# Kernel tuning notes

Hardware: AMD Instinct MI355X
Metric: run time of the kernel (lower is better)

The kernel has to match this reference:

```python
import jax, jax.numpy as jnp
import numpy as np

MARGIN_POS = 0.0
MARGIN_NEG = 1.0
NUM_CLASSES = 1000


def setup_inputs() -> dict:
    key = jax.random.key(0)
    k1, k2, k3, k4, k5 = jax.random.split(key, 5)
    B, D, M = 1024, 512, 32768
    R = M - B  # memory bank length after dedup/truncate
    embeddings = jax.random.normal(k1, (B, D), dtype=jnp.float32)
    labels = jax.random.randint(k2, (B,), 0, NUM_CLASSES).astype(jnp.int64)
    emb_mem = jax.random.normal(k3, (R, D), dtype=jnp.float32)
    # offset so memory labels are disjoint from batch labels (torch.isin dedup is a no-op)
    lbl_mem = (jax.random.randint(k4, (R,), 0, NUM_CLASSES) + NUM_CLASSES).astype(jnp.int64)
    add_to_mem = jax.random.randint(k5, (B,), 0, 2).astype(bool)
    return {"embeddings": embeddings, "labels": labels, "emb_mem": emb_mem,
            "lbl_mem": lbl_mem, "add_to_mem": add_to_mem}


def _loss(embeddings, labels, emb_mem, lbl_mem):
    B = embeddings.shape[0]
    # reference set = detached batch embeddings ++ memory bank (both are constants w.r.t. grad)
    ref_e = jax.lax.stop_gradient(jnp.concatenate([embeddings, emb_mem], axis=0))  # [R, D]
    ref_l = jnp.concatenate([labels, lbl_mem], axis=0)                              # [R]
    idx_ref = jnp.concatenate([jnp.arange(B, dtype=labels.dtype),
                               -jnp.ones(lbl_mem.shape[0], dtype=labels.dtype)])    # [R]
    # squared L2 distance matrix [B, R] via (|a|^2 + |b|^2 - 2 a.b), clamped at 0
    sq_a = jnp.sum(embeddings * embeddings, axis=1)  # [B]
    sq_b = jnp.sum(ref_e * ref_e, axis=1)            # [R]
    d = jnp.maximum(sq_a[:, None] + sq_b[None, :] - 2.0 * (embeddings @ ref_e.T), 0.0)
    not_self = idx_ref[None, :] != jnp.arange(B, dtype=labels.dtype)[:, None]  # [B, R]
    same = labels[:, None] == ref_l[None, :]                                   # [B, R]
    loss_ap = d - MARGIN_POS
    loss_an = jnp.maximum(MARGIN_NEG - d, 0.0)
    mask_pos = same & not_self & (loss_ap > 0)
    mask_neg = (~same) & not_self & (loss_an > 0)
    eps = 1e-6
    loss_pos = (jnp.where(mask_pos, loss_ap, 0.0).sum(1)
                / (mask_pos.sum(1).astype(d.dtype) + eps)).sum()
    loss_neg = (jnp.where(mask_neg, loss_an, 0.0).sum(1)
                / (mask_neg.sum(1).astype(d.dtype) + eps)).sum()
    return (loss_pos + loss_neg) / B


def reference(embeddings, labels, emb_mem, lbl_mem, add_to_mem):
    # add_to_mem only affects the (stateful) memory-bank update, not the returned loss
    return _loss(embeddings, labels, emb_mem, lbl_mem)
```

## Files before the change

kernel.cpp:

```cpp
#include <hip/hip_runtime.h>

typedef __attribute__((ext_vector_type(8))) short short8;
typedef __attribute__((ext_vector_type(4))) float f32x4;

#define GLOAD16(g, l)                                                        \
  __builtin_amdgcn_global_load_lds(                                          \
      (const __attribute__((address_space(1))) unsigned int*)(g),            \
      (__attribute__((address_space(3))) unsigned int*)(l), 16, 0, 0)

__device__ __forceinline__ unsigned short f2bf(float f) {
  union { float f; unsigned int u; } v;
  v.f = f;
  unsigned int u = v.u;
  u += 0x7FFFu + ((u >> 16) & 1u);
  return (unsigned short)(u >> 16);
}

__device__ __forceinline__ short8 pack8(float4 a, float4 b) {
  short8 r;
  r[0] = (short)f2bf(a.x); r[1] = (short)f2bf(a.y);
  r[2] = (short)f2bf(a.z); r[3] = (short)f2bf(a.w);
  r[4] = (short)f2bf(b.x); r[5] = (short)f2bf(b.y);
  r[6] = (short)f2bf(b.z); r[7] = (short)f2bf(b.w);
  return r;
}

#define BM 128
#define BN 128
#define BK 32

__global__ __launch_bounds__(256)
void prep2_kernel(const float* __restrict__ emb, const int* __restrict__ labels,
                  const float* __restrict__ emb_mem, const int* __restrict__ lbl_mem,
                  unsigned short* __restrict__ refbf, float* __restrict__ sqb,
                  int* __restrict__ reflab, float* __restrict__ facc,
                  int* __restrict__ fcnt, int Bn, int Dn, int Mn) {
  if (blockIdx.x == 0 && threadIdx.x == 0) { *facc = 0.f; *fcnt = 0; }
  int wid = threadIdx.x >> 6, lane = threadIdx.x & 63;
  int row = blockIdx.x * 4 + wid;
  if (row >= Mn) return;
  const float* src = (row < Bn) ? (emb + (size_t)row * Dn)
                                : (emb_mem + (size_t)(row - Bn) * Dn);
  unsigned short* dst = refbf + (size_t)row * Dn;
  float s = 0.f;
  for (int c0 = lane * 8; c0 < Dn; c0 += 64 * 8) {
    float4 v0 = ((const float4*)(src + c0))[0];
    float4 v1 = ((const float4*)(src + c0))[1];
    s += v0.x * v0.x + v0.y * v0.y + v0.z * v0.z + v0.w * v0.w;
    s += v1.x * v1.x + v1.y * v1.y + v1.z * v1.z + v1.w * v1.w;
    *(short8*)(dst + c0) = pack8(v0, v1);
  }
#pragma unroll
  for (int off = 32; off; off >>= 1) s += __shfl_xor(s, off);
  if (lane == 0) {
    sqb[row] = s;
    reflab[row] = (row < Bn) ? labels[row] : lbl_mem[row - Bn];
  }
}

__global__ __launch_bounds__(256, 2)
void gemm512x2_kernel(const unsigned short* __restrict__ refbf,
                      const float* __restrict__ sqb,
                      const int* __restrict__ reflab,
                      float* __restrict__ part) {
  __shared__ __align__(16) char smem[32768];
  unsigned short* As = (unsigned short*)smem;
  unsigned short* Bs = (unsigned short*)(smem + 8192);
  f32x4* red4 = (f32x4*)smem;

  const int npart = 128;
  int bid = blockIdx.x;
  int c = bid & 7, g = bid >> 3;
  int jp = c * 16 + (g >> 3);
  int it = g & 7;
  int rowBase = it * BM, colBase = jp * 256;

  int tid = threadIdx.x, lane = tid & 63, w = tid >> 6;
  int wr = w >> 1, wc = w & 1;
  int l16 = lane & 15, quad = lane >> 4;
  int lrow = lane >> 2, lk = lane & 3;

  int ra = w * 32 + lrow;
  int caa = (lk - (ra >> 1)) & 3;
  const char* gA0 = (const char*)refbf + (size_t)(rowBase + ra) * 1024 + caa * 16;
  const char* gA1 = gA0 + 16 * 1024;
  char* lA = (char*)As + w * 2048;
  int rb = w * 64 + lrow;
  int cab = (lk - (rb >> 1)) & 3;
  const char* gB0 = (const char*)refbf + (size_t)(colBase + rb) * 1024 + cab * 16;
  const char* gB1 = gB0 + 16 * 1024;
  const char* gB2 = gB0 + 32 * 1024;
  const char* gB3 = gB0 + 48 * 1024;
  char* lB = (char*)Bs + w * 4096;

  f32x4 acc[4][8] = {};
  for (int kk = 0; kk < 16; ++kk) {
    int ko = kk * 64;
    GLOAD16(gA0 + ko, lA);
    GLOAD16(gA1 + ko, lA + 1024);
    GLOAD16(gB0 + ko, lB);
    GLOAD16(gB1 + ko, lB + 1024);
    GLOAD16(gB2 + ko, lB + 2048);
    GLOAD16(gB3 + ko, lB + 3072);
    __syncthreads();
    short8 af[4], bfr[8];
#pragma unroll
    for (int mi = 0; mi < 4; ++mi) {
      int row = wr * 64 + mi * 16 + l16;
      af[mi] = *(const short8*)&As[row * BK + ((quad + (row >> 1)) & 3) * 8];
    }
#pragma unroll
    for (int ni = 0; ni < 8; ++ni) {
      int row = wc * 128 + ni * 16 + l16;
      bfr[ni] = *(const short8*)&Bs[row * BK + ((quad + (row >> 1)) & 3) * 8];
    }
#pragma unroll
    for (int mi = 0; mi < 4; ++mi)
#pragma unroll
      for (int ni = 0; ni < 8; ++ni)
        acc[mi][ni] = __builtin_amdgcn_mfma_f32_16x16x32_bf16(
            af[mi], bfr[ni], acc[mi][ni], 0, 0, 0);
    __syncthreads();
  }

  float sqc[8];
  int labc[8];
#pragma unroll
  for (int ni = 0; ni < 8; ++ni) {
    int gcol = colBase + wc * 128 + ni * 16 + l16;
    sqc[ni] = sqb[gcol];
    labc[ni] = reflab[gcol];
  }
#pragma unroll
  for (int mi = 0; mi < 4; ++mi) {
    int lr0 = wr * 64 + mi * 16 + quad * 4;
#pragma unroll
    for (int r = 0; r < 4; ++r) {
      int lrl = lr0 + r;
      int grow = rowBase + lrl;
      float sqr = sqb[grow];
      int labr = reflab[grow];
      float ps = 0.f, ns = 0.f, cpk = 0.f;
#pragma unroll
      for (int ni = 0; ni < 8; ++ni) {
        int gcol = colBase + wc * 128 + ni * 16 + l16;
        float dist = fmaxf(sqr + sqc[ni] - 2.0f * acc[mi][ni][r], 0.f);
        bool self = (gcol == grow);
        bool same = (labc[ni] == labr);
        if (same && !self && dist > 0.f) { ps += dist; cpk += 1.f; }
        if (!same && !self && dist < 1.f) { ns += 1.f - dist; cpk += 512.f; }
      }
      ps += __shfl_xor(ps, 8);
      ns += __shfl_xor(ns, 8);
      cpk += __shfl_xor(cpk, 8);
      if (l16 < 8) {
        f32x4 v = {ps, ns, cpk, 0.f};
        red4[(wc * BM + lrl) * 8 + l16] = v;
      }
    }
  }
  __syncthreads();
  if (tid < BM) {
    f32x4 s = {0.f, 0.f, 0.f, 0.f};
#pragma unroll
    for (int c2 = 0; c2 < 2; ++c2)
#pragma unroll
      for (int k = 0; k < 8; ++k)
        s += red4[(c2 * BM + tid) * 8 + ((k + tid) & 7)];
    float nc = floorf(s[2] * (1.0f / 512.0f));
    float pc = s[2] - 512.f * nc;
    f32x4 o = {s[0], pc, s[1], nc};
    ((f32x4*)part)[(size_t)(rowBase + tid) * npart + jp] = o;
  }
}

__global__ __launch_bounds__(256)
void gemm_generic_kernel(const unsigned short* __restrict__ refbf,
                         const float* __restrict__ sqb,
                         const int* __restrict__ reflab,
                         float* __restrict__ part,
                         int Dn, int mtiles, int ntiles) {
  __shared__ unsigned short As[BM * BK];
  __shared__ unsigned short Bs[BN * BK];
  __shared__ f32x4 redbuf4[2 * BM];

  int bid = blockIdx.x;
  int it = bid % mtiles, jt = bid / mtiles;
  int rowBase = it * BM, colBase = jt * BN;
  int tid = threadIdx.x, lane = tid & 63, w = tid >> 6;
  int wr = w >> 1, wc = w & 1;
  int l16 = lane & 15, quad = lane >> 4;
  int lrow = lane >> 2, lk = lane & 3;
  size_t rowB = (size_t)Dn * 2;
  int r0 = w * 32 + lrow;
  int ca = (lk - (r0 >> 1)) & 3;
  const char* gA0 = (const char*)refbf + (size_t)(rowBase + r0) * rowB + ca * 16;
  const char* gA1 = gA0 + 16 * rowB;
  const char* gB0 = (const char*)refbf + (size_t)(colBase + r0) * rowB + ca * 16;
  const char* gB1 = gB0 + 16 * rowB;
  char* lA = (char*)As + w * 2048;
  char* lB = (char*)Bs + w * 2048;

  f32x4 acc[4][4] = {};
  for (int k0 = 0; k0 < Dn; k0 += BK) {
    int koff = k0 * 2;
    GLOAD16(gA0 + koff, lA);
    GLOAD16(gA1 + koff, lA + 1024);
    GLOAD16(gB0 + koff, lB);
    GLOAD16(gB1 + koff, lB + 1024);
    __syncthreads();
    short8 af[4], bfr[4];
#pragma unroll
    for (int mi = 0; mi < 4; ++mi) {
      int row = wr * 64 + mi * 16 + l16;
      af[mi] = *(const short8*)&As[row * BK + ((quad + (row >> 1)) & 3) * 8];
    }
#pragma unroll
    for (int ni = 0; ni < 4; ++ni) {
      int row = wc * 64 + ni * 16 + l16;
      bfr[ni] = *(const short8*)&Bs[row * BK + ((quad + (row >> 1)) & 3) * 8];
    }
#pragma unroll
    for (int mi = 0; mi < 4; ++mi)
#pragma unroll
      for (int ni = 0; ni < 4; ++ni)
        acc[mi][ni] = __builtin_amdgcn_mfma_f32_16x16x32_bf16(
            af[mi], bfr[ni], acc[mi][ni], 0, 0, 0);
    __syncthreads();
  }

  float sqc[4];
  int labc[4];
#pragma unroll
  for (int ni = 0; ni < 4; ++ni) {
    int gcol = colBase + wc * 64 + ni * 16 + l16;
    sqc[ni] = sqb[gcol];
    labc[ni] = reflab[gcol];
  }
#pragma unroll
  for (int mi = 0; mi < 4; ++mi) {
    int lr0 = wr * 64 + mi * 16 + quad * 4;
#pragma unroll
    for (int r = 0; r < 4; ++r) {
      int lrl = lr0 + r;
      int grow = rowBase + lrl;
      float sqr = sqb[grow];
      int labr = reflab[grow];
      float ps = 0.f, pc = 0.f, ns = 0.f, nc = 0.f;
#pragma unroll
      for (int ni = 0; ni < 4; ++ni) {
        int gcol = colBase + wc * 64 + ni * 16 + l16;
        float dist = fmaxf(sqr + sqc[ni] - 2.0f * acc[mi][ni][r], 0.f);
        bool self = (gcol == grow);
        bool same = (labc[ni] == labr);
        if (same && !self && dist > 0.f) { ps += dist; pc += 1.f; }
        if (!same && !self && dist < 1.f) { ns += 1.f - dist; nc += 1.f; }
      }
#pragma unroll
      for (int off = 8; off; off >>= 1) {
        ps += __shfl_xor(ps, off);
        pc += __shfl_xor(pc, off);
        ns += __shfl_xor(ns, off);
        nc += __shfl_xor(nc, off);
      }
      if (l16 == 0) {
        f32x4 v = {ps, pc, ns, nc};
        redbuf4[wc * BM + lrl] = v;
      }
    }
  }
  __syncthreads();
  if (tid < BM) {
    f32x4 s = redbuf4[tid] + redbuf4[BM + tid];
    ((f32x4*)part)[(size_t)(rowBase + tid) * ntiles + jt] = s;
  }
}

__global__ __launch_bounds__(256)
void reduce_final_kernel(const float* __restrict__ part,
                         float* __restrict__ facc, int* __restrict__ fcnt,
                         float* __restrict__ out, int Bn, int npart) {
  __shared__ float rsum[4];
  int tid = threadIdx.x, w = tid >> 6, lane = tid & 63;
  int row = blockIdx.x * 4 + w;
  const f32x4* part4 = (const f32x4*)part;
  float rl = 0.f;
  if (row < Bn) {
    f32x4 a = {0.f, 0.f, 0.f, 0.f};
    for (int j = lane; j < npart; j += 64)
      a += part4[(size_t)row * npart + j];
#pragma unroll
    for (int off = 32; off; off >>= 1) {
      a[0] += __shfl_xor(a[0], off);
      a[1] += __shfl_xor(a[1], off);
      a[2] += __shfl_xor(a[2], off);
      a[3] += __shfl_xor(a[3], off);
    }
    rl = a[0] / (a[1] + 1e-6f) + a[2] / (a[3] + 1e-6f);
  }
  if (lane == 0) rsum[w] = rl;
  __syncthreads();
  if (tid == 0) {
    float bs = rsum[0] + rsum[1] + rsum[2] + rsum[3];
    atomicAdd(facc, bs);
    __threadfence();
    int old = atomicAdd(fcnt, 1);
    if (old == (int)gridDim.x - 1) {
      __threadfence();
      float tot = atomicAdd(facc, 0.f);
      out[0] = tot / (float)Bn;
    }
  }
}

extern "C" void kernel_launch(void* const* d_in, const int* in_sizes, int n_in,
                              void* d_out, int out_size, void* d_ws, size_t ws_size,
                              hipStream_t stream) {
  const float* emb     = (const float*)d_in[0];
  const int*   labels  = (const int*)d_in[1];
  const float* emb_mem = (const float*)d_in[2];
  const int*   lbl_mem = (const int*)d_in[3];

  int Bn = in_sizes[1];
  int Dn = in_sizes[0] / Bn;
  int Rn = in_sizes[3];
  int Mn = Bn + Rn;
  int mtiles = Bn / BM, ntiles = Mn / BN;

  char* ws = (char*)d_ws;
  unsigned short* refbf = (unsigned short*)ws;
  size_t off = (size_t)Mn * Dn * 2;
  float* sqb    = (float*)(ws + off);
  int*   reflab = (int*)(ws + off + (size_t)Mn * 4);
  float* part   = (float*)(ws + off + (size_t)Mn * 8);
  float* facc   = part + (size_t)Bn * ntiles * 4;
  int*   fcnt   = (int*)(facc + 1);

  prep2_kernel<<<(Mn + 3) / 4, 256, 0, stream>>>(
      emb, labels, emb_mem, lbl_mem, refbf, sqb, reflab, facc, fcnt, Bn, Dn, Mn);

  bool fast = (Dn == 512 && mtiles == 8 && ntiles == 256);
  if (fast) {
    gemm512x2_kernel<<<1024, 256, 0, stream>>>(refbf, sqb, reflab, part);
    reduce_final_kernel<<<(Bn + 3) / 4, 256, 0, stream>>>(
        part, facc, fcnt, (float*)d_out, Bn, 128);
  } else {
    gemm_generic_kernel<<<mtiles * ntiles, 256, 0, stream>>>(
        refbf, sqb, reflab, part, Dn, mtiles, ntiles);
    reduce_final_kernel<<<(Bn + 3) / 4, 256, 0, stream>>>(
        part, facc, fcnt, (float*)d_out, Bn, ntiles);
  }
}
```

Before: 160.2 us.

## Double-buffer LDS tiles in fast GEMM to overlap loads with MFMA

Splits the fast-path GEMM's shared memory into two buffers and prefetches the next K-slice with global_load_lds while MFMAs run on the current one. The aim is to hide global-to-LDS latency behind compute. LDS use grows to 48KB per block, which may limit occupancy, and the K loop is now fully unrolled. Correctness depends on the sync still remaining at the end of each iteration, which falls in the unshown part of the loop.

Measured after the change: 162.2 us. About the same (+1.2%).

```diff
diff --git a/kernel.cpp b/kernel.cpp
--- a/kernel.cpp
+++ b/kernel.cpp
@@ -59,13 +59,11 @@
 }
 
 __global__ __launch_bounds__(256, 2)
-void gemm512x2_kernel(const unsigned short* __restrict__ refbf,
-                      const float* __restrict__ sqb,
-                      const int* __restrict__ reflab,
-                      float* __restrict__ part) {
-  __shared__ __align__(16) char smem[32768];
-  unsigned short* As = (unsigned short*)smem;
-  unsigned short* Bs = (unsigned short*)(smem + 8192);
+void gemm512x2db_kernel(const unsigned short* __restrict__ refbf,
+                        const float* __restrict__ sqb,
+                        const int* __restrict__ reflab,
+                        float* __restrict__ part) {
+  __shared__ __align__(16) char smem[49152];
   f32x4* red4 = (f32x4*)smem;
 
   const int npart = 128;
@@ -84,35 +82,50 @@
   int caa = (lk - (ra >> 1)) & 3;
   const char* gA0 = (const char*)refbf + (size_t)(rowBase + ra) * 1024 + caa * 16;
   const char* gA1 = gA0 + 16 * 1024;
-  char* lA = (char*)As + w * 2048;
   int rb = w * 64 + lrow;
   int cab = (lk - (rb >> 1)) & 3;
   const char* gB0 = (const char*)refbf + (size_t)(colBase + rb) * 1024 + cab * 16;
   const char* gB1 = gB0 + 16 * 1024;
   const char* gB2 = gB0 + 32 * 1024;
   const char* gB3 = gB0 + 48 * 1024;
-  char* lB = (char*)Bs + w * 4096;
+
+  char* lA[2] = {smem + w * 2048, smem + 24576 + w * 2048};
+  char* lB[2] = {smem + 8192 + w * 4096, smem + 24576 + 8192 + w * 4096};
 
   f32x4 acc[4][8] = {};
+
+  GLOAD16(gA0, lA[0]);
+  GLOAD16(gA1, lA[0] + 1024);
+  GLOAD16(gB0, lB[0]);
+  GLOAD16(gB1, lB[0] + 1024);
+  GLOAD16(gB2, lB[0] + 2048);
+  GLOAD16(gB3, lB[0] + 3072);
+  __syncthreads();
+
+#pragma unroll
   for (int kk = 0; kk < 16; ++kk) {
-    int ko = kk * 64;
-    GLOAD16(gA0 + ko, lA);
-    GLOAD16(gA1 + ko, lA + 1024);
-    GLOAD16(gB0 + ko, lB);
-    GLOAD16(gB1 + ko, lB + 1024);
-    GLOAD16(gB2 + ko, lB + 2048);
-    GLOAD16(gB3 + ko, lB + 3072);
-    __syncthreads();
+    int cur = kk & 1, nxt = cur ^ 1;
+    if (kk < 15) {
+      int ko = (kk + 1) * 64;
+      GLOAD16(gA0 + ko, lA[nxt]);
+      GLOAD16(gA1 + ko, lA[nxt] + 1024);
+      GLOAD16(gB0 + ko, lB[nxt]);
+      GLOAD16(gB1 + ko, lB[nxt] + 1024);
+      GLOAD16(gB2 + ko, lB[nxt] + 2048);
+      GLOAD16(gB3 + ko, lB[nxt] + 3072);
+    }
+    const unsigned short* Asc = (const unsigned short*)(smem + cur * 24576);
+    const unsigned short* Bsc = (const unsigned short*)(smem + cur * 24576 + 8192);
     short8 af[4], bfr[8];
 #pragma unroll
     for (int mi = 0; mi < 4; ++mi) {
       int row = wr * 64 + mi * 16 + l16;
-      af[mi] = *(const short8*)&As[row * BK + ((quad + (row >> 1)) & 3) * 8];
+      af[mi] = *(const short8*)&Asc[row * BK + ((quad + (row >> 1)) & 3) * 8];
     }
 #pragma unroll
     for (int ni = 0; ni < 8; ++ni) {
       int row = wc * 128 + ni * 16 + l16;
-      bfr[ni] = *(const short8*)&Bs[row * BK + ((quad + (row >> 1)) & 3) * 8];
+      bfr[ni] = *(const short8*)&Bsc[row * BK + ((quad + (row >> 1)) & 3) * 8];
     }
 #pragma unroll
     for (int mi = 0; mi < 4; ++mi)
@@ -341,7 +354,7 @@
 
   bool fast = (Dn == 512 && mtiles == 8 && ntiles == 256);
   if (fast) {
-    gemm512x2_kernel<<<1024, 256, 0, stream>>>(refbf, sqb, reflab, part);
+    gemm512x2db_kernel<<<1024, 256, 0, stream>>>(refbf, sqb, reflab, part);
     reduce_final_kernel<<<(Bn + 3) / 4, 256, 0, stream>>>(
         part, facc, fcnt, (float*)d_out, Bn, 128);
   } else {
```
